# Kernel optimization log

Hardware: AMD Instinct MI355X
Metric: run time of the kernel (lower is better)

The kernel has to match this reference:

```python
import jax, jax.numpy as jnp
import numpy as np

S = 8192
Q_PARAM = 256
V_PARAM = 256
SCALE = 1.0 / np.sqrt(float(Q_PARAM)).astype(np.float32)


def setup_inputs() -> dict:
    key = jax.random.key(0)
    ks = jax.random.split(key, 12)
    init = lambda k, shape, fan_in: jax.random.uniform(k, shape, jnp.float32, -1.0, 1.0) / np.sqrt(float(fan_in))
    return {
        "query": jax.random.normal(ks[0], (S, Q_PARAM), jnp.float32),
        "key": jax.random.normal(ks[1], (S, Q_PARAM), jnp.float32),
        "value": jax.random.normal(ks[2], (S, V_PARAM), jnp.float32),
        "mask": jax.random.uniform(ks[3], (S, S), jnp.float32),
        "Wq": init(ks[4], (Q_PARAM, Q_PARAM), Q_PARAM),
        "bq": init(ks[5], (Q_PARAM,), Q_PARAM),
        "Wk": init(ks[6], (Q_PARAM, Q_PARAM), Q_PARAM),
        "bk": init(ks[7], (Q_PARAM,), Q_PARAM),
        "Wv": init(ks[8], (V_PARAM, V_PARAM), V_PARAM),
        "bv": init(ks[9], (V_PARAM,), V_PARAM),
        "Wo": init(ks[10], (V_PARAM, V_PARAM), V_PARAM),
        "bo": init(ks[11], (V_PARAM,), V_PARAM),
    }


def reference(query, key, value, mask, Wq, bq, Wk, bk, Wv, bv, Wo, bo):
    # torch nn.Linear: y = x @ W.T + b
    q = query @ Wq.T + bq          # [S, q]
    k = key @ Wk.T + bk            # [S, q]
    v = value @ Wv.T + bv          # [S, v]
    scores = q @ k.T               # [S, S]
    masked = scores * mask         # multiplicative mask BEFORE softmax
    h = jax.nn.softmax(masked * SCALE, axis=1)
    h = h @ v                      # [S, v]
    return h @ Wo.T + bo
```

## Files before the change

### kernel.cpp

```cpp
#include <hip/hip_runtime.h>


#define S 8192
#define BM 128
#define BN 32

typedef unsigned short ushort_t;
typedef __attribute__((ext_vector_type(8))) __bf16 bf16x8;
typedef __attribute__((ext_vector_type(4))) float f32x4;
typedef __attribute__((ext_vector_type(4))) ushort_t ushort4_t;
typedef __attribute__((ext_vector_type(8))) ushort_t ushort8_t;
typedef __attribute__((ext_vector_type(4))) unsigned uint4_t;

typedef const __attribute__((address_space(1))) unsigned int* gas_u32;
typedef __attribute__((address_space(3))) unsigned int* las_u32;

__device__ __forceinline__ ushort_t f2bf(float f) {
  unsigned u = __builtin_bit_cast(unsigned, f);
  u += 0x7FFFu + ((u >> 16) & 1u);
  return (ushort_t)(u >> 16);
}

__device__ __forceinline__ bf16x8 pack8(f32x4 a, f32x4 b) {
  ushort8_t u;
  u[0] = f2bf(a[0]); u[1] = f2bf(a[1]); u[2] = f2bf(a[2]); u[3] = f2bf(a[3]);
  u[4] = f2bf(b[0]); u[5] = f2bf(b[1]); u[6] = f2bf(b[2]); u[7] = f2bf(b[3]);
  return __builtin_bit_cast(bf16x8, u);
}

__device__ __forceinline__ unsigned cvt_pk_bf16(float lo, float hi) {
  unsigned r;
  asm("v_cvt_pk_bf16_f32 %0, %1, %2" : "=v"(r) : "v"(lo), "v"(hi));
  return r;
}

__global__ __launch_bounds__(256) void wconv_kernel(
    const float* __restrict__ w0, const float* __restrict__ w1,
    const float* __restrict__ w2, const float* __restrict__ w3,
    ushort_t* __restrict__ o0, ushort_t* __restrict__ o1,
    ushort_t* __restrict__ o2, ushort_t* __restrict__ o3) {
  const int m = blockIdx.y;
  const float* w = (m == 0) ? w0 : (m == 1) ? w1 : (m == 2) ? w2 : w3;
  ushort_t* o = (m == 0) ? o0 : (m == 1) ? o1 : (m == 2) ? o2 : o3;
  const int idx = (blockIdx.x * 256 + threadIdx.x) * 4;
  f32x4 v = *(const f32x4*)(w + idx);
  ushort4_t p;
  p[0] = f2bf(v[0]); p[1] = f2bf(v[1]); p[2] = f2bf(v[2]); p[3] = f2bf(v[3]);
  *(ushort4_t*)(o + idx) = p;
}

__global__ __launch_bounds__(256) void qkv_kernel(
    const float* __restrict__ query, const float* __restrict__ key,
    const float* __restrict__ value,
    const ushort_t* __restrict__ Wqb, const ushort_t* __restrict__ Wkb,
    const ushort_t* __restrict__ Wvb,
    const float* __restrict__ bq, const float* __restrict__ bk,
    const float* __restrict__ bv,
    ushort_t* __restrict__ qo, ushort_t* __restrict__ ko,
    ushort_t* __restrict__ vto) {
  __shared__ __align__(16) ushort_t tb[64 * 68];
  const int z = blockIdx.z;
  const float* inp = (z == 0) ? query : (z == 1) ? key : value;
  const ushort_t* Wb = (z == 0) ? Wqb : (z == 1) ? Wkb : Wvb;
  const float* bias = (z == 0) ? bq : (z == 1) ? bk : bv;

  const int tid = threadIdx.x;
  const int lane = tid & 63;
  const int w = tid >> 6;
  const int lr = lane & 15, lg = lane >> 4;
  const int brow0 = blockIdx.x * 64;
  const int row0 = brow0 + w * 16;
  const int col0 = blockIdx.y * 64;

  f32x4 acc[4] = {};
  const int arow = row0 + lr;
  const int kb = lg * 8;

  bf16x8 af[8];
#pragma unroll
  for (int ks = 0; ks < 8; ++ks) {
    const float* ap = inp + (size_t)arow * 256 + ks * 32 + kb;
    af[ks] = pack8(*(const f32x4*)ap, *(const f32x4*)(ap + 4));
  }
#pragma unroll
  for (int ks = 0; ks < 8; ++ks) {
#pragma unroll
    for (int n = 0; n < 4; ++n) {
      bf16x8 bb = *(const bf16x8*)(Wb + (size_t)(col0 + 16 * n + lr) * 256 + ks * 32 + kb);
      acc[n] = __builtin_amdgcn_mfma_f32_16x16x32_bf16(af[ks], bb, acc[n], 0, 0, 0);
    }
  }

  if (z < 2) {
    ushort_t* o = z ? ko : qo;
#pragma unroll
    for (int n = 0; n < 4; ++n) {
      const int col = col0 + 16 * n + lr;
      const float bv_ = bias[col];
      const int rbase = row0 + lg * 4;
#pragma unroll
      for (int r = 0; r < 4; ++r)
        o[(size_t)(rbase + r) * 256 + col] = f2bf(acc[n][r] + bv_);
    }
  } else {
#pragma unroll
    for (int n = 0; n < 4; ++n) {
      const int col = col0 + 16 * n + lr;
      const float bv_ = bias[col];
      const int cl = 16 * n + lr;
      const int rowl = w * 16 + lg * 4;
      ushort4_t pk;
#pragma unroll
      for (int r = 0; r < 4; ++r) pk[r] = f2bf(acc[n][r] + bv_);
      *(ushort4_t*)&tb[cl * 68 + rowl] = pk;
    }
    __syncthreads();
#pragma unroll
    for (int i = 0; i < 4; ++i) {
      int chunk = i * 256 + tid;
      int c = chunk >> 4;
      int off = (chunk & 15) * 4;
      ushort4_t v0 = *(const ushort4_t*)&tb[c * 68 + off];
      *(ushort4_t*)(vto + (size_t)(col0 + c) * S + brow0 + off) = v0;
    }
  }
}

__global__ __launch_bounds__(256) void oproj_kernel(const ushort_t* __restrict__ inp,
                                                    const ushort_t* __restrict__ Wb,
                                                    const float* __restrict__ bias,
                                                    float* __restrict__ outp) {
  const int tid = threadIdx.x;
  const int lane = tid & 63;
  const int w = tid >> 6;
  const int lr = lane & 15, lg = lane >> 4;
  const int row0 = blockIdx.x * 64 + w * 16;
  const int col0 = blockIdx.y * 64;

  f32x4 acc[4] = {};
  const int arow = row0 + lr;
  const int kb = lg * 8;
#pragma unroll
  for (int ks = 0; ks < 8; ++ks) {
    bf16x8 a = *(const bf16x8*)(inp + (size_t)arow * 256 + ks * 32 + kb);
#pragma unroll
    for (int n = 0; n < 4; ++n) {
      bf16x8 bb = *(const bf16x8*)(Wb + (size_t)(col0 + 16 * n + lr) * 256 + ks * 32 + kb);
      acc[n] = __builtin_amdgcn_mfma_f32_16x16x32_bf16(a, bb, acc[n], 0, 0, 0);
    }
  }
#pragma unroll
  for (int n = 0; n < 4; ++n) {
    const int col = col0 + 16 * n + lr;
    const float bv = bias[col];
    const int rbase = row0 + lg * 4;
#pragma unroll
    for (int r = 0; r < 4; ++r)
      outp[(size_t)(rbase + r) * 256 + col] = acc[n][r] + bv;
  }
}

template <int NS>
__global__ __launch_bounds__(256, 2) void flash_kernel(
    const ushort_t* __restrict__ qg, const ushort_t* __restrict__ kbm,
    const ushort_t* __restrict__ vtb, const float* __restrict__ mask,
    float* __restrict__ Opart, float* __restrict__ lpart) {
  constexpr int KSPL = S / NS;
  constexpr int NT = KSPL / BN;
  __shared__ __align__(16) ushort_t kt[2][BN * 256];
  __shared__ __align__(16) ushort_t vt[2][256 * BN];

  const int tid = threadIdx.x;
  const int lane = tid & 63;
  const int w = tid >> 6;
  const int lr = lane & 15, lg = lane >> 4;
  const int split = blockIdx.y;
  const int kvbase = split * KSPL;
  const int qrow0 = blockIdx.x * BM + w * 32;

  bf16x8 qf[2][8];
#pragma unroll
  for (int qb = 0; qb < 2; ++qb)
#pragma unroll
    for (int ks = 0; ks < 8; ++ks)
      qf[qb][ks] = *(const bf16x8*)(qg + (size_t)(qrow0 + qb * 16 + lr) * 256 + ks * 32 + lg * 8);

  const float* mrow[2];
#pragma unroll
  for (int qb = 0; qb < 2; ++qb)
    mrow[qb] = mask + (size_t)(qrow0 + qb * 16 + lr) * S + lg * 4;

  f32x4 oacc[2][16] = {};
  float lsum[2] = {0.f, 0.f};
  const int vt_swz = ((lg ^ (lr & 3)) << 4);

  auto stage = [&](int b, int kv0) {
#pragma unroll
    for (int it = 0; it < 4; ++it) {
      int chunk = it * 256 + (w << 6) + lane;
      int r = chunk >> 5;
      int c = (chunk & 31) ^ (r & 7);
      const ushort_t* src = kbm + (size_t)(kv0 + r) * 256 + c * 8;
      __builtin_amdgcn_global_load_lds((gas_u32)src,
                                       (las_u32)(&kt[b][0] + it * 2048 + w * 512), 16, 0, 0);
    }
#pragma unroll
    for (int it = 0; it < 4; ++it) {
      int chunk = it * 256 + (w << 6) + lane;
      int r = chunk >> 2;
      int c = (chunk & 3) ^ (r & 3);
      const ushort_t* src = vtb + (size_t)r * S + kv0 + c * 8;
      __builtin_amdgcn_global_load_lds((gas_u32)src,
                                       (las_u32)(&vt[b][0] + it * 2048 + w * 512), 16, 0, 0);
    }
  };

  stage(0, kvbase);
  f32x4 mcur[2][2];
#pragma unroll
  for (int qb = 0; qb < 2; ++qb)
#pragma unroll
    for (int kb = 0; kb < 2; ++kb)
      mcur[qb][kb] = __builtin_nontemporal_load((const f32x4*)(mrow[qb] + kvbase + kb * 16));
  asm volatile("s_waitcnt vmcnt(4)" ::: "memory");
  __builtin_amdgcn_s_barrier();
  __builtin_amdgcn_sched_barrier(0);

  for (int t = 0; t < NT; ++t) {
    const int cur = t & 1;
    const int kvn = kvbase + ((t + 1 < NT) ? (t + 1) : t) * BN;

    stage(cur ^ 1, kvn);

    f32x4 sacc[2][2] = {};
    __builtin_amdgcn_s_setprio(1);
#pragma unroll
    for (int ks = 0; ks < 8; ++ks) {
#pragma unroll
      for (int kb = 0; kb < 2; ++kb) {
        int addr = ((kb * 16 + lr) << 9) + ((((ks << 2) + lg) ^ (lr & 7)) << 4);
        bf16x8 kf = *(const bf16x8*)((const char*)&kt[cur][0] + addr);
#pragma unroll
        for (int qb = 0; qb < 2; ++qb)
          sacc[qb][kb] = __builtin_amdgcn_mfma_f32_16x16x32_bf16(kf, qf[qb][ks], sacc[qb][kb], 0, 0, 0);
      }
    }
    __builtin_amdgcn_s_setprio(0);

    unsigned pw[2][2][2];
#pragma unroll
    for (int qb = 0; qb < 2; ++qb) {
      float p[8];
#pragma unroll
      for (int kb = 0; kb < 2; ++kb)
#pragma unroll
        for (int r = 0; r < 4; ++r) {
          float pv = __builtin_amdgcn_exp2f(sacc[qb][kb][r] * (mcur[qb][kb][r] * 0.09016844005556021f));
          p[kb * 4 + r] = pv;
          lsum[qb] += pv;
        }
      pw[qb][0][0] = cvt_pk_bf16(p[0], p[1]);
      pw[qb][0][1] = cvt_pk_bf16(p[2], p[3]);
      pw[qb][1][0] = cvt_pk_bf16(p[4], p[5]);
      pw[qb][1][1] = cvt_pk_bf16(p[6], p[7]);
    }

#pragma unroll
    for (int qb = 0; qb < 2; ++qb)
#pragma unroll
      for (int kb = 0; kb < 2; ++kb)
        mcur[qb][kb] = __builtin_nontemporal_load((const f32x4*)(mrow[qb] + kvn + kb * 16));

    bf16x8 pfrag[2];
#pragma unroll
    for (int qb = 0; qb < 2; ++qb) {
      unsigned a0 = pw[qb][0][0], a1 = pw[qb][0][1];
      unsigned b0 = pw[qb][1][0], b1 = pw[qb][1][1];
      asm("v_permlane32_swap_b32 %0, %1" : "+v"(a0), "+v"(b0));
      asm("v_permlane16_swap_b32 %0, %1" : "+v"(a0), "+v"(b0));
      asm("v_permlane32_swap_b32 %0, %1" : "+v"(a1), "+v"(b1));
      asm("v_permlane16_swap_b32 %0, %1" : "+v"(a1), "+v"(b1));
      uint4_t u = {a0, a1, b0, b1};
      pfrag[qb] = __builtin_bit_cast(bf16x8, u);
    }

    __builtin_amdgcn_s_setprio(1);
#pragma unroll
    for (int nd = 0; nd < 16; ++nd) {
      bf16x8 va = *(const bf16x8*)((const char*)&vt[cur][0] + nd * 1024 + lr * 64 + vt_swz);
#pragma unroll
      for (int qb = 0; qb < 2; ++qb)
        oacc[qb][nd] = __builtin_amdgcn_mfma_f32_16x16x32_bf16(va, pfrag[qb], oacc[qb][nd], 0, 0, 0);
    }
    __builtin_amdgcn_s_setprio(0);

    asm volatile("s_waitcnt vmcnt(4)" ::: "memory");
    __builtin_amdgcn_s_barrier();
    __builtin_amdgcn_sched_barrier(0);
  }

#pragma unroll
  for (int qb = 0; qb < 2; ++qb) {
    float v = lsum[qb];
    v += __shfl_xor(v, 16);
    v += __shfl_xor(v, 32);
    if (lane < 16)
      lpart[(size_t)split * S + qrow0 + qb * 16 + lr] = v;
#pragma unroll
    for (int nd = 0; nd < 16; ++nd)
      *(f32x4*)(Opart + ((size_t)split * S + qrow0 + qb * 16 + lr) * 256 + nd * 16 + lg * 4) = oacc[qb][nd];
  }
}

template <int NS>
__global__ __launch_bounds__(256) void combine_kernel(const float* __restrict__ Opart,
                                                      const float* __restrict__ lpart,
                                                      ushort_t* __restrict__ hb) {
  const int row = blockIdx.x;
  const int d = threadIdx.x;
  float L = 0.f, acc = 0.f;
#pragma unroll
  for (int s2 = 0; s2 < NS; ++s2) {
    L += lpart[(size_t)s2 * S + row];
    acc += Opart[((size_t)s2 * S + row) * 256 + d];
  }
  hb[(size_t)row * 256 + d] = f2bf(acc / L);
}

extern "C" void kernel_launch(void* const* d_in, const int* in_sizes, int n_in,
                              void* d_out, int out_size, void* d_ws, size_t ws_size,
                              hipStream_t stream) {
  const float* query = (const float*)d_in[0];
  const float* key   = (const float*)d_in[1];
  const float* value = (const float*)d_in[2];
  const float* mask  = (const float*)d_in[3];
  const float* Wq = (const float*)d_in[4];
  const float* bq = (const float*)d_in[5];
  const float* Wk = (const float*)d_in[6];
  const float* bk = (const float*)d_in[7];
  const float* Wv = (const float*)d_in[8];
  const float* bv = (const float*)d_in[9];
  const float* Wo = (const float*)d_in[10];
  const float* bo = (const float*)d_in[11];

  char* ws = (char*)d_ws;
  ushort_t* qb  = (ushort_t*)(ws);
  ushort_t* kb  = (ushort_t*)(ws + ((size_t)4  << 20));
  ushort_t* vtb = (ushort_t*)(ws + ((size_t)8  << 20));
  ushort_t* hb  = (ushort_t*)(ws + ((size_t)12 << 20));
  ushort_t* Wqb = (ushort_t*)(ws + ((size_t)16 << 20));
  ushort_t* Wkb = (ushort_t*)(ws + ((size_t)16 << 20) + (128u << 10));
  ushort_t* Wvb = (ushort_t*)(ws + ((size_t)16 << 20) + (256u << 10));
  ushort_t* Wob = (ushort_t*)(ws + ((size_t)16 << 20) + (384u << 10));
  float* lpart  = (float*)(ws + ((size_t)16 << 20) + (512u << 10));
  float* Opart  = (float*)(ws + ((size_t)17 << 20));

  const bool big = ws_size >= ((size_t)82 << 20);

  wconv_kernel<<<dim3(64, 4), 256, 0, stream>>>(Wq, Wk, Wv, Wo, Wqb, Wkb, Wvb, Wob);

  qkv_kernel<<<dim3(S / 64, 4, 3), 256, 0, stream>>>(query, key, value,
                                                     Wqb, Wkb, Wvb, bq, bk, bv,
                                                     qb, kb, vtb);

  if (big) {
    flash_kernel<8><<<dim3(S / BM, 8), 256, 0, stream>>>(qb, kb, vtb, mask, Opart, lpart);
    combine_kernel<8><<<S, 256, 0, stream>>>(Opart, lpart, hb);
  } else {
    flash_kernel<4><<<dim3(S / BM, 4), 256, 0, stream>>>(qb, kb, vtb, mask, Opart, lpart);
    combine_kernel<4><<<S, 256, 0, stream>>>(Opart, lpart, hb);
  }

  oproj_kernel<<<dim3(S / 64, 4), 256, 0, stream>>>(hb, Wob, bo, (float*)d_out);
}
```

Baseline: 225.3 us.

## Triple-buffer K/V tiles with register-prefetched K fragments in flash kernel

Moves the flash kernel's K/V LDS staging from double to triple buffering so global-to-LDS loads run two tiles ahead. Next-tile K fragments and all V fragments are prefetched into registers ahead of the MFMA loops, and the loop is unrolled by two to alternate register buffers. Launch bounds drop to one block per SIMD pair and the split is fixed at 4, which removes the 8-split path. The aim is to hide LDS read latency behind MFMAs, at the cost of much higher register and LDS use, lower occupancy, and fewer blocks in flight.

```diff
diff --git a/kernel.cpp b/kernel.cpp
--- a/kernel.cpp
+++ b/kernel.cpp
@@ -160,15 +160,17 @@
   }
 }
 
+struct KF { bf16x8 f[16]; };
+
 template <int NS>
-__global__ __launch_bounds__(256, 2) void flash_kernel(
+__global__ __launch_bounds__(256, 1) void flash_kernel(
     const ushort_t* __restrict__ qg, const ushort_t* __restrict__ kbm,
     const ushort_t* __restrict__ vtb, const float* __restrict__ mask,
     float* __restrict__ Opart, float* __restrict__ lpart) {
   constexpr int KSPL = S / NS;
   constexpr int NT = KSPL / BN;
-  __shared__ __align__(16) ushort_t kt[2][BN * 256];
-  __shared__ __align__(16) ushort_t vt[2][256 * BN];
+  __shared__ __align__(16) ushort_t lk[3][BN * 256];
+  __shared__ __align__(16) ushort_t lv[3][256 * BN];
 
   const int tid = threadIdx.x;
   const int lane = tid & 63;
@@ -194,7 +196,7 @@
   float lsum[2] = {0.f, 0.f};
   const int vt_swz = ((lg ^ (lr & 3)) << 4);
 
-  auto stage = [&](int b, int kv0) {
+  auto stage = [&](int bi, int kv0) {
 #pragma unroll
     for (int it = 0; it < 4; ++it) {
       int chunk = it * 256 + (w << 6) + lane;
@@ -202,7 +204,7 @@
       int c = (chunk & 31) ^ (r & 7);
       const ushort_t* src = kbm + (size_t)(kv0 + r) * 256 + c * 8;
       __builtin_amdgcn_global_load_lds((gas_u32)src,
-                                       (las_u32)(&kt[b][0] + it * 2048 + w * 512), 16, 0, 0);
+                                       (las_u32)(&lk[bi][0] + it * 2048 + w * 512), 16, 0, 0);
     }
 #pragma unroll
     for (int it = 0; it < 4; ++it) {
@@ -211,40 +213,61 @@
       int c = (chunk & 3) ^ (r & 3);
       const ushort_t* src = vtb + (size_t)r * S + kv0 + c * 8;
       __builtin_amdgcn_global_load_lds((gas_u32)src,
-                                       (las_u32)(&vt[b][0] + it * 2048 + w * 512), 16, 0, 0);
+                                       (las_u32)(&lv[bi][0] + it * 2048 + w * 512), 16, 0, 0);
     }
   };
 
+  auto ld_k = [&](KF& kf, int bi) {
+#pragma unroll
+    for (int ks = 0; ks < 8; ++ks)
+#pragma unroll
+      for (int kb = 0; kb < 2; ++kb) {
+        int addr = ((kb * 16 + lr) << 9) + ((((ks << 2) + lg) ^ (lr & 7)) << 4);
+        kf.f[ks * 2 + kb] = *(const bf16x8*)((const char*)&lk[bi][0] + addr);
+      }
+  };
+
+  f32x4 mcur[2][2];
+  auto ld_mask = [&](int kv0) {
+#pragma unroll
+    for (int qb = 0; qb < 2; ++qb)
+#pragma unroll
+      for (int kb = 0; kb < 2; ++kb)
+        mcur[qb][kb] = __builtin_nontemporal_load((const f32x4*)(mrow[qb] + kv0 + kb * 16));
+  };
+
+  KF kfA, kfB;
+
   stage(0, kvbase);
-  f32x4 mcur[2][2];
-#pragma unroll
-  for (int qb = 0; qb < 2; ++qb)
-#pragma unroll
-    for (int kb = 0; kb < 2; ++kb)
-      mcur[qb][kb] = __builtin_nontemporal_load((const f32x4*)(mrow[qb] + kvbase + kb * 16));
+  stage(1, kvbase + BN);
+  ld_mask(kvbase);
   asm volatile("s_waitcnt vmcnt(4)" ::: "memory");
   __builtin_amdgcn_s_barrier();
   __builtin_amdgcn_sched_barrier(0);
-
-  for (int t = 0; t < NT; ++t) {
-    const int cur = t & 1;
+  ld_k(kfA, 0);
+
+  auto body = [&](int t, KF& kU, KF& kL) {
+    const int cur = t % 3, nxt = (t + 1) % 3, stg = (t + 2) % 3;
     const int kvn = kvbase + ((t + 1 < NT) ? (t + 1) : t) * BN;
 
-    stage(cur ^ 1, kvn);
+    if (t + 2 < NT) stage(stg, kvbase + (t + 2) * BN);
+
+    bf16x8 vf[16];
+#pragma unroll
+    for (int nd = 0; nd < 16; ++nd)
+      vf[nd] = *(const bf16x8*)((const char*)&lv[cur][0] + nd * 1024 + lr * 64 + vt_swz);
+
+    if (t + 1 < NT) ld_k(kL, nxt);
 
     f32x4 sacc[2][2] = {};
     __builtin_amdgcn_s_setprio(1);
 #pragma unroll
-    for (int ks = 0; ks < 8; ++ks) {
-#pragma unroll
-      for (int kb = 0; kb < 2; ++kb) {
-        int addr = ((kb * 16 + lr) << 9) + ((((ks << 2) + lg) ^ (lr & 7)) << 4);
-        bf16x8 kf = *(const bf16x8*)((const char*)&kt[cur][0] + addr);
+    for (int ks = 0; ks < 8; ++ks)
+#pragma unroll
+      for (int kb = 0; kb < 2; ++kb)
 #pragma unroll
         for (int qb = 0; qb < 2; ++qb)
-          sacc[qb][kb] = __builtin_amdgcn_mfma_f32_16x16x32_bf16(kf, qf[qb][ks], sacc[qb][kb], 0, 0, 0);
-      }
-    }
+          sacc[qb][kb] = __builtin_amdgcn_mfma_f32_16x16x32_bf16(kU.f[ks * 2 + kb], qf[qb][ks], sacc[qb][kb], 0, 0, 0);
     __builtin_amdgcn_s_setprio(0);
 
     unsigned pw[2][2][2];
@@ -265,11 +288,7 @@
       pw[qb][1][1] = cvt_pk_bf16(p[6], p[7]);
     }
 
-#pragma unroll
-    for (int qb = 0; qb < 2; ++qb)
-#pragma unroll
-      for (int kb = 0; kb < 2; ++kb)
-        mcur[qb][kb] = __builtin_nontemporal_load((const f32x4*)(mrow[qb] + kvn + kb * 16));
+    ld_mask(kvn);
 
     bf16x8 pfrag[2];
 #pragma unroll
@@ -286,17 +305,20 @@
 
     __builtin_amdgcn_s_setprio(1);
 #pragma unroll
-    for (int nd = 0; nd < 16; ++nd) {
-      bf16x8 va = *(const bf16x8*)((const char*)&vt[cur][0] + nd * 1024 + lr * 64 + vt_swz);
+    for (int nd = 0; nd < 16; ++nd)
 #pragma unroll
       for (int qb = 0; qb < 2; ++qb)
-        oacc[qb][nd] = __builtin_amdgcn_mfma_f32_16x16x32_bf16(va, pfrag[qb], oacc[qb][nd], 0, 0, 0);
-    }
+        oacc[qb][nd] = __builtin_amdgcn_mfma_f32_16x16x32_bf16(vf[nd], pfrag[qb], oacc[qb][nd], 0, 0, 0);
     __builtin_amdgcn_s_setprio(0);
 
     asm volatile("s_waitcnt vmcnt(4)" ::: "memory");
     __builtin_amdgcn_s_barrier();
     __builtin_amdgcn_sched_barrier(0);
+  };
+
+  for (int t = 0; t < NT; t += 2) {
+    body(t, kfA, kfB);
+    body(t + 1, kfB, kfA);
   }
 
 #pragma unroll
@@ -355,21 +377,15 @@
   float* lpart  = (float*)(ws + ((size_t)16 << 20) + (512u << 10));
   float* Opart  = (float*)(ws + ((size_t)17 << 20));
 
-  const bool big = ws_size >= ((size_t)82 << 20);
-
   wconv_kernel<<<dim3(64, 4), 256, 0, stream>>>(Wq, Wk, Wv, Wo, Wqb, Wkb, Wvb, Wob);
 
   qkv_kernel<<<dim3(S / 64, 4, 3), 256, 0, stream>>>(query, key, value,
                                                      Wqb, Wkb, Wvb, bq, bk, bv,
                                                      qb, kb, vtb);
 
-  if (big) {
-    flash_kernel<8><<<dim3(S / BM, 8), 256, 0, stream>>>(qb, kb, vtb, mask, Opart, lpart);
-    combine_kernel<8><<<S, 256, 0, stream>>>(Opart, lpart, hb);
-  } else {
-    flash_kernel<4><<<dim3(S / BM, 4), 256, 0, stream>>>(qb, kb, vtb, mask, Opart, lpart);
-    combine_kernel<4><<<S, 256, 0, stream>>>(Opart, lpart, hb);
-  }
+  flash_kernel<4><<<dim3(S / BM, 4), 256, 0, stream>>>(qb, kb, vtb, mask, Opart, lpart);
+
+  combine_kernel<4><<<S, 256, 0, stream>>>(Opart, lpart, hb);
 
   oproj_kernel<<<dim3(S / 64, 4), 256, 0, stream>>>(hb, Wob, bo, (float*)d_out);
 }
```

Result: slower. 288.8 us (+28.2%).
